# Kernel tuning notes

Measured on AMD Instinct MI355X. Metric: run time of the kernel, lower is better.

Reference implementation:

```python
import jax, jax.numpy as jnp
import numpy as np
import math

D_MODEL = 2048
NUM_HEADS = 32
NUM_KV_HEADS = 8
D_K = D_MODEL // NUM_HEADS  # 64
GROUPS = NUM_HEADS // NUM_KV_HEADS  # 4
WINDOW = 512
ROPE_BASE = 10000.0


def setup_inputs() -> dict:
    key = jax.random.key(0)
    ks = jax.random.split(key, 5)
    B, T = 2, 2048
    x = jax.random.normal(ks[0], (B, T, D_MODEL), dtype=jnp.float32)
    s = 0.02  # typical init scale to keep logits sane
    Wq = jax.random.normal(ks[1], (D_MODEL, D_MODEL), dtype=jnp.float32) * s
    Wk = jax.random.normal(ks[2], (NUM_KV_HEADS * D_K, D_MODEL), dtype=jnp.float32) * s
    Wv = jax.random.normal(ks[3], (NUM_KV_HEADS * D_K, D_MODEL), dtype=jnp.float32) * s
    Wo = jax.random.normal(ks[4], (D_MODEL, D_MODEL), dtype=jnp.float32) * s
    return {"x": x, "Wq": Wq, "Wk": Wk, "Wv": Wv, "Wo": Wo}


def _rotate_half(t):
    half = t.shape[-1] // 2
    return jnp.concatenate([-t[..., half:], t[..., :half]], axis=-1)


def _rope_cos_sin(T, dtype):
    inv_freq = 1.0 / (ROPE_BASE ** (jnp.arange(0, D_K, 2, dtype=jnp.float32) / D_K))
    pos = jnp.arange(T, dtype=jnp.float32)
    freqs = pos[:, None] * inv_freq[None, :]            # [T, D_K/2]
    emb = jnp.concatenate([freqs, freqs], axis=-1)       # [T, D_K]
    return jnp.cos(emb).astype(dtype)[None, None], jnp.sin(emb).astype(dtype)[None, None]


def reference(x, Wq, Wk, Wv, Wo):
    B, T, D = x.shape
    # Projections (nn.Linear: x @ W.T)
    Q = (x @ Wq.T).reshape(B, T, NUM_HEADS, D_K).transpose(0, 2, 1, 3)     # [B,H,T,dk]
    K = (x @ Wk.T).reshape(B, T, NUM_KV_HEADS, D_K).transpose(0, 2, 1, 3)  # [B,KV,T,dk]
    V = (x @ Wv.T).reshape(B, T, NUM_KV_HEADS, D_K).transpose(0, 2, 1, 3)
    # RoPE
    cos, sin = _rope_cos_sin(T, x.dtype)
    Q = Q * cos + _rotate_half(Q) * sin
    K = K * cos + _rotate_half(K) * sin
    # GQA: fold group dim into Q instead of repeat_interleave on K/V (same math)
    Qg = Q.reshape(B, NUM_KV_HEADS, GROUPS, T, D_K)
    scale = math.sqrt(D_K)
    scores = jnp.einsum('bhgqd,bhkd->bhgqk', Qg, K) / scale  # [B,KV,G,T,T]
    # sliding-window causal mask: valid iff 0 <= q_pos - k_pos < WINDOW
    pos = jnp.arange(T)
    dist = pos[:, None] - pos[None, :]
    win_mask = (dist < 0) | (dist >= WINDOW)
    scores = jnp.where(win_mask[None, None, None], -jnp.inf, scores)
    attn = jax.nn.softmax(scores, axis=-1)
    out = jnp.einsum('bhgqk,bhkd->bhgqd', attn, V)
    out = out.reshape(B, NUM_HEADS, T, D_K).transpose(0, 2, 1, 3).reshape(B, T, D)
    return out @ Wo.T
```

## Files before the change

### kernel.cpp

```cpp
#include <hip/hip_runtime.h>
#include <hip/hip_bf16.h>
#include <cstdint>
#include <cstddef>

typedef __attribute__((ext_vector_type(4))) float f32x4;
typedef __attribute__((ext_vector_type(8))) short bf16x8;
typedef __attribute__((ext_vector_type(4))) int i32x4;
typedef void __attribute__((address_space(1)))* as1_void_p;
typedef void __attribute__((address_space(3)))* as3_void_p;

#define T_SEQ 2048
#define D_MODEL 2048
#define NUM_HEADS 32
#define NUM_KV 8
#define GROUPS 4
#define DK 64
#define WINDOW 512
#define BATCH 2

#define NEG_BIG (-30000.0f)

__device__ __forceinline__ unsigned short f2b(float f) {
    unsigned int u = __builtin_bit_cast(unsigned int, f);
    u = (u + 0x7FFFu + ((u >> 16) & 1u)) >> 16;
    return (unsigned short)u;
}

__device__ __forceinline__ unsigned int cvtpk_bf16(float lo, float hi) {
    unsigned int r;
    asm("v_cvt_pk_bf16_f32 %0, %1, %2" : "=v"(r) : "v"(lo), "v"(hi));
    return r;
}

__device__ __forceinline__ void load_lds16(const void* g, void* l) {
    __builtin_amdgcn_global_load_lds((as1_void_p)(uintptr_t)g,
                                     (as3_void_p)(unsigned int)(uintptr_t)l,
                                     16, 0, 0);
}

#define CAST_N0 8388608
#define CAST_N1 12582912
#define CAST_N2 13631488
#define CAST_N3 14680064
#define CAST_N4 18874368
__global__ void cast_all_kernel(const float* __restrict__ x, const float* __restrict__ wq,
                                const float* __restrict__ wk, const float* __restrict__ wv,
                                const float* __restrict__ wo, unsigned short* __restrict__ dst) {
    int i = (blockIdx.x * blockDim.x + threadIdx.x) * 4;
    const int stride = gridDim.x * blockDim.x * 4;
    for (; i < CAST_N4; i += stride) {
        const float* src;
        int off;
        if (i < CAST_N0)      { src = x;  off = i; }
        else if (i < CAST_N1) { src = wq; off = i - CAST_N0; }
        else if (i < CAST_N2) { src = wk; off = i - CAST_N1; }
        else if (i < CAST_N3) { src = wv; off = i - CAST_N2; }
        else                  { src = wo; off = i - CAST_N3; }
        const float4 v = *(const float4*)(src + off);
        ushort4 o;
        o.x = f2b(v.x); o.y = f2b(v.y); o.z = f2b(v.z); o.w = f2b(v.w);
        *(ushort4*)(dst + i) = o;
    }
}

__global__ void rope_table_kernel(float* __restrict__ ct, float* __restrict__ st) {
    int i = blockIdx.x * blockDim.x + threadIdx.x;
    int t = i >> 5, j = i & 31;
    const float kln = 0.28782313662425556f;
    float inv = __expf(-(float)j * kln);
    if (j == 0) inv = 1.0f;
    float ang = (float)t * inv;
    float s, c;
    sincosf(ang, &s, &c);
    ct[i] = c; st[i] = s;
}

__global__ __launch_bounds__(512, 2) void gemm_qkv_rope(
    const unsigned short* __restrict__ A, const unsigned short* __restrict__ Bw,
    const float* __restrict__ ct, const float* __restrict__ st,
    unsigned short* __restrict__ Qb, unsigned short* __restrict__ Kb,
    unsigned short* __restrict__ Vt) {
    __shared__ __align__(16) unsigned short lds[65536];
    const int bid = blockIdx.x;
    const int xcd = bid & 7;
    const int l = bid >> 3;
    const int stl = l >> 2;
    const int w = l & 3;
    const int tile_m = xcd * 2 + (w >> 1);
    const int tile_n = stl * 2 + (w & 1);

    const int tid = threadIdx.x;
    const int lane = tid & 63;
    const int wid = tid >> 6;
    const int wr = wid >> 2, wc = wid & 3;
    const int lrow = lane & 15;
    const int g = lane >> 4;
    const int arow = tile_m * 256, brow = tile_n * 256;

    f32x4 acc[8][4] = {};

#define QSTAGE(SRC, ROWBASE, KCOL, USHOFF)                                     \
    { _Pragma("unroll") for (int u = 0; u < 2; ++u) {                          \
        const int gi = u * 512 + tid;                                          \
        const int row_ = gi >> 2, sl_ = gi & 3;                                \
        const int sc_ = (sl_ ^ ((row_ >> 1) & 3)) << 3;                        \
        load_lds16(SRC + (size_t)((ROWBASE) + row_) * 2048 + (KCOL) + sc_,     \
                   (char*)&lds[USHOFF] + gi * 16); } }

    QSTAGE(A, arow, 0,  0)     QSTAGE(Bw, brow, 0,  8192)
    QSTAGE(A, arow, 32, 16384) QSTAGE(Bw, brow, 32, 24576)
    QSTAGE(A, arow, 64, 32768) QSTAGE(Bw, brow, 64, 40960)
    asm volatile("s_waitcnt vmcnt(8)" ::: "memory");
    __builtin_amdgcn_sched_barrier(0);
    __builtin_amdgcn_s_barrier();

    for (int t = 0; t < 64; ++t) {
        const int cb = (t & 3) * 16384;
        const int sb = ((t + 3) & 3) * 16384;
        bf16x8 af[8], bfr[4];
#pragma unroll
        for (int m = 0; m < 8; ++m) {
            const int R = wr * 128 + m * 16 + lrow;
            af[m] = *(const bf16x8*)&lds[cb + R * 32 + ((g ^ ((R >> 1) & 3)) << 3)];
        }
#pragma unroll
        for (int n = 0; n < 4; ++n) {
            const int R = wc * 64 + n * 16 + lrow;
            bfr[n] = *(const bf16x8*)&lds[cb + 8192 + R * 32 + ((g ^ ((R >> 1) & 3)) << 3)];
        }
        if (t + 3 < 64) {
            QSTAGE(A, arow, (t + 3) * 32, sb)
            QSTAGE(Bw, brow, (t + 3) * 32, sb + 8192)
        }
        __builtin_amdgcn_s_setprio(1);
#pragma unroll
        for (int m = 0; m < 8; ++m)
#pragma unroll
            for (int n = 0; n < 4; ++n)
                acc[m][n] = __builtin_amdgcn_mfma_f32_16x16x32_bf16(af[m], bfr[n], acc[m][n], 0, 0, 0);
        __builtin_amdgcn_s_setprio(0);
        if (t < 61)      { asm volatile("s_waitcnt vmcnt(8)" ::: "memory"); }
        else if (t == 61){ asm volatile("s_waitcnt vmcnt(4)" ::: "memory"); }
        else             { asm volatile("s_waitcnt vmcnt(0)" ::: "memory"); }
        __builtin_amdgcn_sched_barrier(0);
        __builtin_amdgcn_s_barrier();
    }
#undef QSTAGE

    const int hcol = tile_n * 4 + wc;
#pragma unroll
    for (int m = 0; m < 8; ++m) {
        const int row0 = tile_m * 256 + wr * 128 + m * 16 + g * 4;
        const int bb = row0 >> 11;
        const int t0 = row0 & 2047;
        if (hcol < 40) {
            const bool isQ = (hcol < 32);
            const float sc = isQ ? 0.125f : 1.0f;
            unsigned short* base = isQ
                ? (Qb + ((size_t)(bb * NUM_HEADS + hcol) * T_SEQ) * 64)
                : (Kb + ((size_t)(bb * NUM_KV + (hcol - 32)) * T_SEQ) * 64);
#pragma unroll
            for (int r = 0; r < 4; ++r) {
                const int t = t0 + r;
                unsigned short* dst = base + (size_t)t * 64;
#pragma unroll
                for (int n = 0; n < 2; ++n) {
                    const int j = n * 16 + lrow;
                    const float c = ct[t * 32 + j], s = st[t * 32 + j];
                    const float v0 = acc[m][n][r], v1 = acc[m][n + 2][r];
                    dst[j]      = f2b((v0 * c - v1 * s) * sc);
                    dst[j + 32] = f2b((v1 * c + v0 * s) * sc);
                }
            }
        } else {
            const int vh = hcol - 40;
            const int chunk = t0 >> 5, tk = t0 & 31;
            unsigned short* cbase = Vt + ((size_t)(bb * NUM_KV + vh) * 64 + chunk) * 2048 + tk;
#pragma unroll
            for (int n = 0; n < 4; ++n) {
                const int d = n * 16 + lrow;
                unsigned int u0 = cvtpk_bf16(acc[m][n][0], acc[m][n][1]);
                unsigned int u1 = cvtpk_bf16(acc[m][n][2], acc[m][n][3]);
                uint2 val; val.x = u0; val.y = u1;
                *(uint2*)(cbase + d * 32) = val;
            }
        }
    }
}

__global__ __launch_bounds__(512, 2) void gemm_bf16_nt(
    const unsigned short* __restrict__ A, const unsigned short* __restrict__ B,
    float* __restrict__ C) {
    __shared__ __align__(16) unsigned short lds[49152];
    const int bid = blockIdx.x;
    const int xcd = bid & 7;
    const int l = bid >> 3;
    const int stl = l >> 1;
    const int w = l & 1;
    const int tile_m = xcd * 2 + w;
    const int tile_n = stl;

    const int tid = threadIdx.x;
    const int lane = tid & 63;
    const int wid = tid >> 6;
    const int wr = wid >> 1, wc = wid & 1;
    const int lrow = lane & 15;
    const int g = lane >> 4;
    const int arow = tile_m * 256, brow = tile_n * 128;

    f32x4 acc[4][4] = {};

#define OSTAGE(BUF, KCOL)                                                      \
    {                                                                          \
        _Pragma("unroll") for (int u = 0; u < 2; ++u) {                        \
            const int gi = u * 512 + tid;                                      \
            const int row_ = gi >> 2, sl_ = gi & 3;                            \
            const int sc_ = (sl_ ^ ((row_ >> 1) & 3)) << 3;                    \
            load_lds16(A + (size_t)(arow + row_) * 2048 + (KCOL) + sc_,        \
                       (char*)&lds[(BUF) * 12288] + gi * 16);                  \
        }                                                                      \
        {                                                                      \
            const int row_ = tid >> 2, sl_ = tid & 3;                          \
            const int sc_ = (sl_ ^ ((row_ >> 1) & 3)) << 3;                    \
            load_lds16(B + (size_t)(brow + row_) * 2048 + (KCOL) + sc_,        \
                       (char*)&lds[(BUF) * 12288 + 8192] + tid * 16);          \
        }                                                                      \
    }

    OSTAGE(0, 0) OSTAGE(1, 32) OSTAGE(2, 64)
    asm volatile("s_waitcnt vmcnt(6)" ::: "memory");
    __builtin_amdgcn_sched_barrier(0);
    __builtin_amdgcn_s_barrier();

    for (int t = 0; t < 64; ++t) {
        const int cb = (t & 3) * 12288;
        const int sb = (t + 3) & 3;
        bf16x8 af[4], bfr[4];
#pragma unroll
        for (int m = 0; m < 4; ++m) {
            const int R = wr * 64 + m * 16 + lrow;
            af[m] = *(const bf16x8*)&lds[cb + R * 32 + ((g ^ ((R >> 1) & 3)) << 3)];
        }
#pragma unroll
        for (int n = 0; n < 4; ++n) {
            const int R = wc * 64 + n * 16 + lrow;
            bfr[n] = *(const bf16x8*)&lds[cb + 8192 + R * 32 + ((g ^ ((R >> 1) & 3)) << 3)];
        }
        if (t + 3 < 64) OSTAGE(sb, (t + 3) * 32)
        __builtin_amdgcn_s_setprio(1);
#pragma unroll
        for (int m = 0; m < 4; ++m)
#pragma unroll
            for (int n = 0; n < 4; ++n)
                acc[m][n] = __builtin_amdgcn_mfma_f32_16x16x32_bf16(af[m], bfr[n], acc[m][n], 0, 0, 0);
        __builtin_amdgcn_s_setprio(0);
        if (t < 61)      { asm volatile("s_waitcnt vmcnt(6)" ::: "memory"); }
        else if (t == 61){ asm volatile("s_waitcnt vmcnt(3)" ::: "memory"); }
        else             { asm volatile("s_waitcnt vmcnt(0)" ::: "memory"); }
        __builtin_amdgcn_sched_barrier(0);
        __builtin_amdgcn_s_barrier();
    }
#undef OSTAGE

#pragma unroll
    for (int m = 0; m < 4; ++m)
#pragma unroll
        for (int n = 0; n < 4; ++n) {
            const int col = tile_n * 128 + wc * 64 + n * 16 + lrow;
#pragma unroll
            for (int r = 0; r < 4; ++r) {
                const int row = tile_m * 256 + wr * 64 + m * 16 + g * 4 + r;
                C[(size_t)row * 2048 + col] = acc[m][n][r];
            }
        }
}

__global__ __launch_bounds__(512, 4) void attn_kernel(
    const unsigned short* __restrict__ Qb, const unsigned short* __restrict__ Kb,
    const unsigned short* __restrict__ Vt, unsigned short* __restrict__ Oout) {
    __shared__ __align__(16) unsigned short lds[16384];
    const int tid = threadIdx.x;
    const int lane = tid & 63;
    const int wv = tid >> 6;
    const int g4 = wv & 3;
    const int tile = wv >> 2;
    const int bid = blockIdx.x;
    const int kvh = bid & 7;
    const int b = (bid >> 3) & 1;
    const int band = 63 - (bid >> 4);
    const int q0A = band * 32;
    const int q0w = q0A + tile * 16;
    const int h = kvh * 4 + g4;

    const int lq = lane & 15;
    const int g = lane >> 4;
    const int kq8 = g * 8;
    const int q = q0w + lq;

    const unsigned short* Qrow = Qb + ((size_t)((b * NUM_HEADS + h) * T_SEQ) + q) * 64;
    const bf16x8 qf0 = *(const bf16x8*)(Qrow + kq8);
    const bf16x8 qf1 = *(const bf16x8*)(Qrow + 32 + kq8);

    f32x4 acc[4] = {};
    float lrun = 0.0f;

    int kc_lo = q0A - (WINDOW - 1);
    if (kc_lo < 0) kc_lo = 0;
    kc_lo &= ~31;
    const int N = ((q0A - kc_lo) >> 5) + 1;

    const unsigned short* Kg = Kb + (size_t)(b * NUM_KV + kvh) * T_SEQ * 64
                                  + (size_t)kc_lo * 64;
    const unsigned short* Vg = Vt + (size_t)(b * NUM_KV + kvh) * 64 * T_SEQ
                                  + (size_t)(kc_lo >> 5) * 2048;

    const int perm = (lq >> 2) * 8 + (lq & 3);
#define SWZK(r) (((r & 3) | ((r >> 3) << 2)) & 7)
    const int koff0 = perm * 64 + ((g ^ SWZK(perm)) << 3);
    const int koff1 = perm * 64 + (((4 + g) ^ SWZK(perm)) << 3);
    const int perm4 = perm + 4;
    const int koff2 = perm4 * 64 + ((g ^ SWZK(perm4)) << 3);
    const int koff3 = perm4 * 64 + (((4 + g) ^ SWZK(perm4)) << 3);
    int voff[4];
#pragma unroll
    for (int nd = 0; nd < 4; ++nd)
        voff[nd] = 2048 + (nd * 16 + lq) * 32 + ((g ^ ((lq >> 1) & 3)) << 3);

#define STAGE(T, BUF)                                                          \
    {                                                                          \
        if (tid < 256) {                                                       \
            const int row_ = tid >> 3, ps = tid & 7;                           \
            const int ls = ps ^ SWZK(row_);                                    \
            load_lds16(Kg + (size_t)(T) * 2048 + row_ * 64 + ls * 8,           \
                       (char*)lds + (BUF) * 8192 + tid * 16);                  \
        } else {                                                               \
            const int gi = tid - 256;                                          \
            const int row_ = gi >> 2, ps = gi & 3;                             \
            const int ls = ps ^ ((row_ >> 1) & 3);                             \
            load_lds16(Vg + (size_t)(T) * 2048 + row_ * 32 + ls * 8,           \
                       (char*)lds + (BUF) * 8192 + 4096 + gi * 16);            \
        }                                                                      \
    }

    STAGE(0, 0)
    if (N > 1) STAGE(1, 1)
    if (N > 2) STAGE(2, 2)
    if (N > 2)      { asm volatile("s_waitcnt vmcnt(2)" ::: "memory"); }
    else if (N > 1) { asm volatile("s_waitcnt vmcnt(1)" ::: "memory"); }
    else            { asm volatile("s_waitcnt vmcnt(0)" ::: "memory"); }
    __builtin_amdgcn_sched_barrier(0);
    __builtin_amdgcn_s_barrier();

    for (int t = 0; t < N; ++t) {
        const int kb = (t & 3) * 4096;
        bf16x8 kf[4], vf[4];
        kf[0] = *(const bf16x8*)&lds[kb + koff0];
        kf[1] = *(const bf16x8*)&lds[kb + koff1];
        kf[2] = *(const bf16x8*)&lds[kb + koff2];
        kf[3] = *(const bf16x8*)&lds[kb + koff3];
#pragma unroll
        for (int nd = 0; nd < 4; ++nd) vf[nd] = *(const bf16x8*)&lds[kb + voff[nd]];
        if (t + 3 < N) STAGE(t + 3, (t + 3) & 3)

        const int kc = kc_lo + t * 32;
        f32x4 st2[2] = {};
        st2[0] = __builtin_amdgcn_mfma_f32_16x16x32_bf16(kf[0], qf0, st2[0], 0, 0, 0);
        st2[0] = __builtin_amdgcn_mfma_f32_16x16x32_bf16(kf[1], qf1, st2[0], 0, 0, 0);
        st2[1] = __builtin_amdgcn_mfma_f32_16x16x32_bf16(kf[2], qf0, st2[1], 0, 0, 0);
        st2[1] = __builtin_amdgcn_mfma_f32_16x16x32_bf16(kf[3], qf1, st2[1], 0, 0, 0);

        float s8[8];
#pragma unroll
        for (int tt = 0; tt < 2; ++tt)
#pragma unroll
            for (int r = 0; r < 4; ++r) s8[tt * 4 + r] = st2[tt][r];

        if (kc < q0w - 496 || kc > q0w - 31) {
#pragma unroll
            for (int i = 0; i < 8; ++i) {
                const int key = kc + g * 8 + ((i >> 2) << 2) + (i & 3);
                const int dist = q - key;
                if (dist < 0 || dist >= WINDOW) s8[i] = NEG_BIG;
            }
        }

        float p8[8];
        float ps = 0.0f;
#pragma unroll
        for (int i = 0; i < 8; ++i) {
            p8[i] = __expf(s8[i]);
            ps += p8[i];
        }
        lrun += ps;

        i32x4 pwi;
        pwi[0] = (int)cvtpk_bf16(p8[0], p8[1]);
        pwi[1] = (int)cvtpk_bf16(p8[2], p8[3]);
        pwi[2] = (int)cvtpk_bf16(p8[4], p8[5]);
        pwi[3] = (int)cvtpk_bf16(p8[6], p8[7]);
        const bf16x8 pw = __builtin_bit_cast(bf16x8, pwi);

#pragma unroll
        for (int nd = 0; nd < 4; ++nd)
            acc[nd] = __builtin_amdgcn_mfma_f32_16x16x32_bf16(vf[nd], pw, acc[nd], 0, 0, 0);

        if (t + 1 < N) {
            if (t + 3 < N)      { asm volatile("s_waitcnt vmcnt(2)" ::: "memory"); }
            else if (t + 2 < N) { asm volatile("s_waitcnt vmcnt(1)" ::: "memory"); }
            else                { asm volatile("s_waitcnt vmcnt(0)" ::: "memory"); }
            __builtin_amdgcn_sched_barrier(0);
            __builtin_amdgcn_s_barrier();
        }
    }
#undef STAGE
#undef SWZK

    lrun += __shfl_xor(lrun, 16);
    lrun += __shfl_xor(lrun, 32);

    const float inv = 1.0f / lrun;
#pragma unroll
    for (int nd = 0; nd < 4; ++nd) {
        unsigned int u0 = cvtpk_bf16(acc[nd][0] * inv, acc[nd][1] * inv);
        unsigned int u1 = cvtpk_bf16(acc[nd][2] * inv, acc[nd][3] * inv);
        unsigned short* dst = Oout + ((size_t)(b * T_SEQ + q)) * D_MODEL + h * 64 + nd * 16 + g * 4;
        uint2 val; val.x = u0; val.y = u1;
        *(uint2*)dst = val;
    }
}

extern "C" void kernel_launch(void* const* d_in, const int* in_sizes, int n_in,
                              void* d_out, int out_size, void* d_ws, size_t ws_size,
                              hipStream_t stream) {
    const float* x = (const float*)d_in[0];
    const float* Wq = (const float*)d_in[1];
    const float* Wk = (const float*)d_in[2];
    const float* Wv = (const float*)d_in[3];
    const float* Wo = (const float*)d_in[4];
    float* out = (float*)d_out;

    char* ws = (char*)d_ws;
    size_t off = 0;
    auto alloc = [&](size_t bytes) -> char* {
        char* p = ws + off;
        off += (bytes + 255) & ~(size_t)255;
        return p;
    };
    unsigned short* xb   = (unsigned short*)alloc(8388608ull * 2);
    unsigned short* wcat = (unsigned short*)alloc(6291456ull * 2);
    unsigned short* wob  = (unsigned short*)alloc(4194304ull * 2);
    unsigned short* qb   = (unsigned short*)alloc(8388608ull * 2);
    unsigned short* kb   = (unsigned short*)alloc(2097152ull * 2);
    unsigned short* vt   = (unsigned short*)alloc(2097152ull * 2);
    unsigned short* attn = (unsigned short*)alloc(8388608ull * 2);
    float* ct            = (float*)alloc(65536ull * 4);
    float* st            = (float*)alloc(65536ull * 4);

    cast_all_kernel<<<2048, 256, 0, stream>>>(x, Wq, Wk, Wv, Wo, xb);
    rope_table_kernel<<<256, 256, 0, stream>>>(ct, st);

    gemm_qkv_rope<<<192, 512, 0, stream>>>(xb, wcat, ct, st, qb, kb, vt);

    attn_kernel<<<1024, 512, 0, stream>>>(qb, kb, vt, attn);

    gemm_bf16_nt<<<256, 512, 0, stream>>>(attn, wob, out);
}
```

Before: 149.3 us.

## Load QKV GEMM A operand directly from global into registers, stage only B in LDS

In the QKV projection GEMM, the A (activation) tile is no longer staged through LDS. Each wave now reads its A fragments straight from global memory into registers with per-row pointers, and only the weight tile keeps the 3-deep LDS ring. This halves LDS use and cuts LDS writes and reads for A, which may let more blocks fit per CU. The cost is that waves sharing the same rows now fetch A redundantly from global, and the A loads are issued and waited on in the same iteration, so their latency is no longer hidden by prefetch.

```diff
diff --git a/kernel.cpp b/kernel.cpp
--- a/kernel.cpp
+++ b/kernel.cpp
@@ -80,7 +80,7 @@
     const float* __restrict__ ct, const float* __restrict__ st,
     unsigned short* __restrict__ Qb, unsigned short* __restrict__ Kb,
     unsigned short* __restrict__ Vt) {
-    __shared__ __align__(16) unsigned short lds[65536];
+    __shared__ __align__(16) unsigned short lds[32768];
     const int bid = blockIdx.x;
     const int xcd = bid & 7;
     const int l = bid >> 3;
@@ -99,39 +99,39 @@
 
     f32x4 acc[8][4] = {};
 
-#define QSTAGE(SRC, ROWBASE, KCOL, USHOFF)                                     \
+    const unsigned short* arp[8];
+#pragma unroll
+    for (int m = 0; m < 8; ++m)
+        arp[m] = A + (size_t)(arow + wr * 128 + m * 16 + lrow) * 2048 + g * 8;
+
+#define BSTAGE(KCOL, USHOFF)                                                   \
     { _Pragma("unroll") for (int u = 0; u < 2; ++u) {                          \
         const int gi = u * 512 + tid;                                          \
         const int row_ = gi >> 2, sl_ = gi & 3;                                \
         const int sc_ = (sl_ ^ ((row_ >> 1) & 3)) << 3;                        \
-        load_lds16(SRC + (size_t)((ROWBASE) + row_) * 2048 + (KCOL) + sc_,     \
+        load_lds16(Bw + (size_t)(brow + row_) * 2048 + (KCOL) + sc_,           \
                    (char*)&lds[USHOFF] + gi * 16); } }
 
-    QSTAGE(A, arow, 0,  0)     QSTAGE(Bw, brow, 0,  8192)
-    QSTAGE(A, arow, 32, 16384) QSTAGE(Bw, brow, 32, 24576)
-    QSTAGE(A, arow, 64, 32768) QSTAGE(Bw, brow, 64, 40960)
-    asm volatile("s_waitcnt vmcnt(8)" ::: "memory");
+    BSTAGE(0, 0) BSTAGE(32, 8192) BSTAGE(64, 16384)
+    asm volatile("s_waitcnt vmcnt(4)" ::: "memory");
     __builtin_amdgcn_sched_barrier(0);
     __builtin_amdgcn_s_barrier();
 
     for (int t = 0; t < 64; ++t) {
-        const int cb = (t & 3) * 16384;
-        const int sb = ((t + 3) & 3) * 16384;
-        bf16x8 af[8], bfr[4];
-#pragma unroll
-        for (int m = 0; m < 8; ++m) {
-            const int R = wr * 128 + m * 16 + lrow;
-            af[m] = *(const bf16x8*)&lds[cb + R * 32 + ((g ^ ((R >> 1) & 3)) << 3)];
-        }
+        const int cb = (t & 3) * 8192;
+        bf16x8 af[8];
+#pragma unroll
+        for (int m = 0; m < 8; ++m)
+            af[m] = *(const bf16x8*)(arp[m] + t * 32);
+        bf16x8 bfr[4];
 #pragma unroll
         for (int n = 0; n < 4; ++n) {
             const int R = wc * 64 + n * 16 + lrow;
-            bfr[n] = *(const bf16x8*)&lds[cb + 8192 + R * 32 + ((g ^ ((R >> 1) & 3)) << 3)];
-        }
-        if (t + 3 < 64) {
-            QSTAGE(A, arow, (t + 3) * 32, sb)
-            QSTAGE(Bw, brow, (t + 3) * 32, sb + 8192)
-        }
+            bfr[n] = *(const bf16x8*)&lds[cb + R * 32 + ((g ^ ((R >> 1) & 3)) << 3)];
+        }
+        if (t + 3 < 64) BSTAGE((t + 3) * 32, ((t + 3) & 3) * 8192)
+        if (t <= 60) { asm volatile("s_waitcnt vmcnt(2)" ::: "memory"); }
+        else         { asm volatile("s_waitcnt vmcnt(0)" ::: "memory"); }
         __builtin_amdgcn_s_setprio(1);
 #pragma unroll
         for (int m = 0; m < 8; ++m)
@@ -139,13 +139,10 @@
             for (int n = 0; n < 4; ++n)
                 acc[m][n] = __builtin_amdgcn_mfma_f32_16x16x32_bf16(af[m], bfr[n], acc[m][n], 0, 0, 0);
         __builtin_amdgcn_s_setprio(0);
-        if (t < 61)      { asm volatile("s_waitcnt vmcnt(8)" ::: "memory"); }
-        else if (t == 61){ asm volatile("s_waitcnt vmcnt(4)" ::: "memory"); }
-        else             { asm volatile("s_waitcnt vmcnt(0)" ::: "memory"); }
         __builtin_amdgcn_sched_barrier(0);
         __builtin_amdgcn_s_barrier();
     }
-#undef QSTAGE
+#undef BSTAGE
 
     const int hcol = tile_n * 4 + wc;
 #pragma unroll
```

Result: slower. 244.7 us (+63.9%).
